# Kernel optimization log

Measured on AMD Instinct MI355X. Metric: run time of the kernel, lower is better.

Reference implementation:

```python
import jax, jax.numpy as jnp
import numpy as np

K = 4
EPS = 1e-6
NEG_INF = -1e9


def _extract_patches(x, k):
    # x: [C, H, W] -> [P, C*k*k], P = (H-k+1)*(W-k+1), p = hp*Wp + wp
    C, H, W = x.shape
    Hp, Wp = H - k + 1, W - k + 1
    cols = jnp.stack([x[:, di:di + Hp, dj:dj + Wp]
                      for di in range(k) for dj in range(k)], axis=1)  # [C, k*k, Hp, Wp]
    return cols.reshape(C * k * k, Hp * Wp).T  # [P, C*k*k]


def setup_inputs() -> dict:
    key = jax.random.key(0)
    k1, k2, k3 = jax.random.split(key, 3)
    C, H, W = 32, 80, 80
    low = jax.random.normal(k1, (1, C, H, W), dtype=jnp.float32)
    high = jax.random.normal(k2, (1, C, H, W), dtype=jnp.float32)
    mask = jax.random.randint(k3, (H + 1, W + 1), 0, 2, dtype=jnp.int32)
    return {"low_level_features": low, "hight_level_features": high, "mask": mask}


def reference(low_level_features, hight_level_features, mask):
    k = K
    low = low_level_features[0]    # [C, H, W]
    high = hight_level_features[0]
    C, H, W = low.shape
    Hp, Wp = H - k + 1, W - k + 1
    P = Hp * Wp

    low_p = _extract_patches(low, k)    # [P, D], D = C*k*k (candidate patches)
    high_p = _extract_patches(high, k)  # [P, D] (query filters)
    norms = jnp.sqrt(jnp.sum(low_p * low_p, axis=1))  # torch.norm per patch, [P]

    # all-pairs cosine-distance scores: [P_query, P_candidate]
    scores = jnp.einsum('qd,pd->qp', high_p, low_p) / (norms + EPS)[None, :]
    # candidates where mask==1 (top-left of patch) are excluded (set to inf=-1e9)
    excl = (mask[:Hp, :Wp].reshape(-1) == 1)
    scores = jnp.where(excl[None, :], NEG_INF, scores)
    best = jnp.argmax(scores, axis=1)   # [P] best match per query patch

    # a query patch at (i,j) is processed only if its 4 mask corners are nonzero
    valid = ((mask[:Hp, :Wp] != 0) & (mask[:Hp, k:k + Wp] != 0) &
             (mask[k:k + Hp, :Wp] != 0) & (mask[k:k + Hp, k:k + Wp] != 0))
    validf = valid.astype(low.dtype).reshape(-1)  # [P]

    gathered = low_p[best] * validf[:, None]            # [P, D]
    g = gathered.reshape(Hp, Wp, C, k, k)               # per-query result patches
    vmap2d = validf.reshape(Hp, Wp)

    result = jnp.zeros_like(low)
    counts = jnp.zeros((H, W), low.dtype)
    for di in range(k):
        for dj in range(k):
            result = result.at[:, di:di + Hp, dj:dj + Wp].add(
                jnp.moveaxis(g[:, :, :, di, dj], -1, 0))
            counts = counts.at[di:di + Hp, dj:dj + Wp].add(vmap2d)

    out = result / (counts + EPS)[None, :, :]
    nz = counts != 0
    out = out * nz[None, :, :] + low * (~nz)[None, :, :]
    return out[None]  # [1, C, H, W]
```

## Files before the change

kernel.cpp:

```cpp
#include <hip/hip_runtime.h>
#include <hip/hip_bf16.h>

#define CC    32
#define HH    80
#define WW    80
#define HW    6400
#define HPQ   77
#define WPQ   77
#define PP    5929
#define DD    512
#define MSTR  81
#define NTILE 93
#define QTILES 372
#define NEGINF (-1e9f)

typedef __attribute__((ext_vector_type(4))) float f32x4;
typedef __attribute__((ext_vector_type(8))) short bf16x8;
typedef __attribute__((ext_vector_type(8))) unsigned short u16x8;

__device__ __forceinline__ void split_bf16(float v, unsigned short& hi, unsigned short& lo) {
    __hip_bfloat16 h = __float2bfloat16(v);
    float hf = __bfloat162float(h);
    __hip_bfloat16 lw = __float2bfloat16(v - hf);
    hi = *reinterpret_cast<unsigned short*>(&h);
    lo = *reinterpret_cast<unsigned short*>(&lw);
}

__global__ __launch_bounds__(1024) void k_mask(const int* __restrict__ mask,
                                               int* __restrict__ excl,
                                               int* __restrict__ valid,
                                               int* __restrict__ qlist,
                                               int* __restrict__ nvalid) {
    __shared__ int cnt;
    if (threadIdx.x == 0) cnt = 0;
    __syncthreads();
    for (int p = threadIdx.x; p < PP; p += 1024) {
        int pi = p / WPQ, pj = p % WPQ;
        int m00 = mask[pi * MSTR + pj];
        int m01 = mask[pi * MSTR + pj + 4];
        int m10 = mask[(pi + 4) * MSTR + pj];
        int m11 = mask[(pi + 4) * MSTR + pj + 4];
        excl[p] = (m00 == 1) ? 1 : 0;
        int v = (m00 != 0 && m01 != 0 && m10 != 0 && m11 != 0) ? 1 : 0;
        valid[p] = v;
        if (v) {
            int s = atomicAdd(&cnt, 1);
            qlist[s] = p;
        }
    }
    __syncthreads();
    if (threadIdx.x == 0) *nvalid = cnt;
}

__global__ __launch_bounds__(256) void k_packBn(const float* __restrict__ low,
                                                unsigned short* __restrict__ Bhi,
                                                unsigned short* __restrict__ Blo) {
    const int u = blockIdx.x;
    const int tid = threadIdx.x;
    const int l = tid & 63, w = tid >> 6;
    const int n = l & 15, quad = l >> 4;
    const int p = u * 16 + n;
    const bool pok = (p < PP);
    const int pi = pok ? p / WPQ : 0, pj = pok ? p % WPQ : 0;
    const int pbase = pi * WW + pj;

    float v[4][8];
    float sq = 0.f;
#pragma unroll
    for (int ss = 0; ss < 4; ++ss) {
        int s = w * 4 + ss;
        int kbase = s * 32 + quad * 8;
        int base = (kbase >> 4) * HW + pbase;
#pragma unroll
        for (int j = 0; j < 8; ++j) {
            int kk = kbase + j;
            int di = (kk >> 2) & 3, dj = kk & 3;
            float x = pok ? low[base + di * WW + dj] : 0.f;
            v[ss][j] = x;
            sq += x * x;
        }
    }
    __shared__ float part[16][17];
    __shared__ float invn_s[16];
    part[w * 4 + quad][n] = sq;
    __syncthreads();
    if (tid < 16) {
        float t = 0.f;
#pragma unroll
        for (int i = 0; i < 16; ++i) t += part[i][tid];
        invn_s[tid] = 1.0f / (sqrtf(t) + 1e-6f);
    }
    __syncthreads();
    const float sc = invn_s[n];
#pragma unroll
    for (int ss = 0; ss < 4; ++ss) {
        int s = w * 4 + ss;
        u16x8 vh, vl;
#pragma unroll
        for (int j = 0; j < 8; ++j) {
            unsigned short h, lo;
            split_bf16(v[ss][j] * sc, h, lo);
            vh[j] = h; vl[j] = lo;
        }
        int off = u * 8192 + s * 512 + l * 8;
        *reinterpret_cast<u16x8*>(Bhi + off) = vh;
        *reinterpret_cast<u16x8*>(Blo + off) = vl;
    }
}

__global__ __launch_bounds__(256) void k_packA(const float* __restrict__ high,
                                               const int* __restrict__ qlist,
                                               const int* __restrict__ nvalid,
                                               unsigned short* __restrict__ Ahi,
                                               unsigned short* __restrict__ Alo) {
    int t = blockIdx.x * 256 + threadIdx.x;
    if (t >= QTILES * 16 * 64) return;
    int nv = *nvalid;
    int l = t & 63;
    int s = (t >> 6) & 15;
    int u = t >> 10;
    if ((u >> 2) * 64 >= nv) return;
    int m = l & 15, quad = l >> 4;
    int slot = u * 16 + m;
    int kbase = s * 32 + quad * 8;

    u16x8 vh, vl;
    if (slot < nv) {
        int q = qlist[slot];
        int qi = q / WPQ, qj = q % WPQ;
        int base = (kbase >> 4) * HW + qi * WW + qj;
#pragma unroll
        for (int j = 0; j < 8; ++j) {
            int kk = kbase + j;
            int di = (kk >> 2) & 3, dj = kk & 3;
            float v = high[base + di * WW + dj];
            unsigned short h, lo;
            split_bf16(v, h, lo);
            vh[j] = h; vl[j] = lo;
        }
    } else {
#pragma unroll
        for (int j = 0; j < 8; ++j) { vh[j] = 0; vl[j] = 0; }
    }
    int off = t * 8;
    *reinterpret_cast<u16x8*>(Ahi + off) = vh;
    *reinterpret_cast<u16x8*>(Alo + off) = vl;
}

__global__ __launch_bounds__(256) void k_score(const unsigned short* __restrict__ Ahi,
                                               const unsigned short* __restrict__ Alo,
                                               const unsigned short* __restrict__ Bhi,
                                               const unsigned short* __restrict__ Blo,
                                               const int* __restrict__ excl,
                                               const int* __restrict__ nvalid,
                                               float* __restrict__ pscore,
                                               int* __restrict__ pidx) {
    const int nv = *nvalid;
    const int qblk = blockIdx.y;
    if (qblk * 64 >= nv) return;
    const int pblk = blockIdx.x;
    const int w = threadIdx.x >> 6;
    const int l = threadIdx.x & 63;
    const int qtile = qblk * 4 + w;

    f32x4 acc[4];
#pragma unroll
    for (int pt = 0; pt < 4; ++pt) acc[pt] = (f32x4){0.f, 0.f, 0.f, 0.f};

    const int abase = qtile * 8192 + l * 8;
    const int bbase0 = pblk * 4 * 8192 + l * 8;

#pragma unroll 4
    for (int s = 0; s < 16; ++s) {
        bf16x8 ah = *reinterpret_cast<const bf16x8*>(Ahi + abase + s * 512);
        bf16x8 al = *reinterpret_cast<const bf16x8*>(Alo + abase + s * 512);
#pragma unroll
        for (int pt = 0; pt < 4; ++pt) {
            int boff = bbase0 + pt * 8192 + s * 512;
            bf16x8 bh = *reinterpret_cast<const bf16x8*>(Bhi + boff);
            bf16x8 bl = *reinterpret_cast<const bf16x8*>(Blo + boff);
            acc[pt] = __builtin_amdgcn_mfma_f32_16x16x32_bf16(ah, bh, acc[pt], 0, 0, 0);
            acc[pt] = __builtin_amdgcn_mfma_f32_16x16x32_bf16(ah, bl, acc[pt], 0, 0, 0);
            acc[pt] = __builtin_amdgcn_mfma_f32_16x16x32_bf16(al, bh, acc[pt], 0, 0, 0);
        }
    }

    const int n = l & 15, quad = l >> 4;
    float bs[4]; int bi[4];
#pragma unroll
    for (int r = 0; r < 4; ++r) { bs[r] = -3.4e38f; bi[r] = 0x7fffffff; }
#pragma unroll
    for (int pt = 0; pt < 4; ++pt) {
        int gp = pblk * 64 + pt * 16 + n;
        if (gp < PP) {
            bool ex = (excl[gp] != 0);
#pragma unroll
            for (int r = 0; r < 4; ++r) {
                float sv = ex ? NEGINF : acc[pt][r];
                if (sv > bs[r]) { bs[r] = sv; bi[r] = gp; }
            }
        }
    }
#pragma unroll
    for (int off = 1; off <= 8; off <<= 1) {
#pragma unroll
        for (int r = 0; r < 4; ++r) {
            float s2 = __shfl_xor(bs[r], off, 64);
            int   i2 = __shfl_xor(bi[r], off, 64);
            if (s2 > bs[r] || (s2 == bs[r] && i2 < bi[r])) { bs[r] = s2; bi[r] = i2; }
        }
    }
    if (n == 0) {
#pragma unroll
        for (int r = 0; r < 4; ++r) {
            int slot = qtile * 16 + quad * 4 + r;
            pscore[slot * NTILE + pblk] = bs[r];
            pidx[slot * NTILE + pblk] = bi[r];
        }
    }
}

__global__ __launch_bounds__(64) void k_reduce(const float* __restrict__ pscore,
                                               const int* __restrict__ pidx,
                                               const int* __restrict__ qlist,
                                               const int* __restrict__ nvalid,
                                               int* __restrict__ best) {
    const int slot = blockIdx.x;
    if (slot >= *nvalid) return;
    const int t = threadIdx.x;
    float bs = -3.4e38f;
    int bi = 0x7fffffff;
    for (int k = t; k < NTILE; k += 64) {
        float s = pscore[slot * NTILE + k];
        int i = pidx[slot * NTILE + k];
        if (s > bs || (s == bs && i < bi)) { bs = s; bi = i; }
    }
#pragma unroll
    for (int off = 32; off >= 1; off >>= 1) {
        float s2 = __shfl_down(bs, off);
        int   i2 = __shfl_down(bi, off);
        if (s2 > bs || (s2 == bs && i2 < bi)) { bs = s2; bi = i2; }
    }
    if (t == 0) best[qlist[slot]] = bi;
}

__global__ __launch_bounds__(256) void k_prep(const int* __restrict__ best,
                                              const int* __restrict__ valid,
                                              int* __restrict__ cnt,
                                              int* __restrict__ offlist) {
    int pix = blockIdx.x * 256 + threadIdx.x;
    if (pix >= HW) return;
    int i = pix / WW, j = pix % WW;
    int n = 0;
#pragma unroll
    for (int di = 0; di < 4; ++di) {
        int qi = i - di;
        if (qi < 0 || qi >= HPQ) continue;
#pragma unroll
        for (int dj = 0; dj < 4; ++dj) {
            int qj = j - dj;
            if (qj < 0 || qj >= WPQ) continue;
            int q = qi * WPQ + qj;
            if (valid[q]) {
                int b = best[q];
                int bi = b / WPQ, bj = b % WPQ;
                offlist[pix * 16 + n] = (bi + di) * WW + (bj + dj);
                n++;
            }
        }
    }
    cnt[pix] = n;
}

__global__ __launch_bounds__(256) void k_out(const float* __restrict__ low,
                                             const int* __restrict__ cnt,
                                             const int* __restrict__ offlist,
                                             float* __restrict__ out) {
    int idx = blockIdx.x * 256 + threadIdx.x;
    if (idx >= CC * HW) return;
    int c = idx / HW;
    int pix = idx % HW;
    int n = cnt[pix];
    if (n > 0) {
        int base = c * HW;
        float acc = 0.f;
        for (int t = 0; t < n; ++t)
            acc += low[base + offlist[pix * 16 + t]];
        out[idx] = acc / ((float)n + 1e-6f);
    } else {
        out[idx] = low[idx];
    }
}

extern "C" void kernel_launch(void* const* d_in, const int* in_sizes, int n_in,
                              void* d_out, int out_size, void* d_ws, size_t ws_size,
                              hipStream_t stream) {
    const float* low  = (const float*)d_in[0];
    const float* high = (const float*)d_in[1];
    const int*   mask = (const int*)d_in[2];
    float* out = (float*)d_out;

    char* ws = (char*)d_ws;
    int*   nvalid = (int*)(ws);
    int*   qlist  = (int*)(ws + 64);
    int*   excl   = (int*)(ws + 24064);
    int*   valid  = (int*)(ws + 48128);
    int*   best   = (int*)(ws + 72192);
    float* pscore = (float*)(ws + 96256);
    int*   pidx   = (int*)(ws + 2310400);
    int*   cnt    = (int*)(ws + 4524544);
    int*   offlist= (int*)(ws + 4550144);
    unsigned short* Ahi = (unsigned short*)(ws + 4959744);
    unsigned short* Alo = (unsigned short*)(ws + 11054592);
    unsigned short* Bhi = (unsigned short*)(ws + 17149440);
    unsigned short* Blo = (unsigned short*)(ws + 23244288);

    hipLaunchKernelGGL(k_mask, dim3(1), dim3(1024), 0, stream,
                       mask, excl, valid, qlist, nvalid);
    hipLaunchKernelGGL(k_packBn, dim3(QTILES), dim3(256), 0, stream,
                       low, Bhi, Blo);
    hipLaunchKernelGGL(k_packA, dim3(QTILES * 4), dim3(256), 0, stream,
                       high, qlist, nvalid, Ahi, Alo);
    hipLaunchKernelGGL(k_score, dim3(NTILE, 93), dim3(256), 0, stream,
                       Ahi, Alo, Bhi, Blo, excl, nvalid, pscore, pidx);
    hipLaunchKernelGGL(k_reduce, dim3(5952), dim3(64), 0, stream,
                       pscore, pidx, qlist, nvalid, best);
    hipLaunchKernelGGL(k_prep, dim3((HW + 255) / 256), dim3(256), 0, stream,
                       best, valid, cnt, offlist);
    hipLaunchKernelGGL(k_out, dim3((CC * HW + 255) / 256), dim3(256), 0, stream,
                       low, cnt, offlist, out);
}
```

Before: 111.2 us.

## Fuse argmax reduction via packed atomicMax and merge pack/output kernels

Replaces the per-tile partial score/index buffers and separate reduce kernel with a 64-bit packed (order-preserving score, inverted index) atomicMax into a per-slot best array, cleared in the mask kernel. Merges the A and B packing kernels into one launch, and fuses the prep and output gather kernels into one that computes offsets on the fly and handles 8 channels per thread. This cuts the launch count from seven to four and removes intermediate global traffic, at the cost of global atomic contention and recomputing the offsets in each channel group.

```diff
diff --git a/kernel.cpp b/kernel.cpp
--- a/kernel.cpp
+++ b/kernel.cpp
@@ -12,6 +12,7 @@
 #define MSTR  81
 #define NTILE 93
 #define QTILES 372
+#define NSLOT 5952
 #define NEGINF (-1e9f)
 
 typedef __attribute__((ext_vector_type(4))) float f32x4;
@@ -26,13 +27,22 @@
     lo = *reinterpret_cast<unsigned short*>(&lw);
 }
 
+__device__ __forceinline__ unsigned long long enc_si(float s, int idx) {
+    unsigned int b = __float_as_uint(s);
+    unsigned int u = (b & 0x80000000u) ? ~b : (b | 0x80000000u);
+    return ((unsigned long long)u << 32) | (unsigned int)(~idx);
+}
+
 __global__ __launch_bounds__(1024) void k_mask(const int* __restrict__ mask,
                                                int* __restrict__ excl,
                                                int* __restrict__ valid,
                                                int* __restrict__ qlist,
-                                               int* __restrict__ nvalid) {
+                                               int* __restrict__ qslot,
+                                               int* __restrict__ nvalid,
+                                               unsigned long long* __restrict__ bestPacked) {
     __shared__ int cnt;
     if (threadIdx.x == 0) cnt = 0;
+    for (int i = threadIdx.x; i < NSLOT; i += 1024) bestPacked[i] = 0ull;
     __syncthreads();
     for (int p = threadIdx.x; p < PP; p += 1024) {
         int pi = p / WPQ, pj = p % WPQ;
@@ -46,105 +56,107 @@
         if (v) {
             int s = atomicAdd(&cnt, 1);
             qlist[s] = p;
+            qslot[p] = s;
         }
     }
     __syncthreads();
     if (threadIdx.x == 0) *nvalid = cnt;
 }
 
-__global__ __launch_bounds__(256) void k_packBn(const float* __restrict__ low,
-                                                unsigned short* __restrict__ Bhi,
-                                                unsigned short* __restrict__ Blo) {
-    const int u = blockIdx.x;
+__global__ __launch_bounds__(256) void k_pack(const float* __restrict__ low,
+                                              const float* __restrict__ high,
+                                              const int* __restrict__ qlist,
+                                              const int* __restrict__ nvalid,
+                                              unsigned short* __restrict__ Bhi,
+                                              unsigned short* __restrict__ Blo,
+                                              unsigned short* __restrict__ Ahi,
+                                              unsigned short* __restrict__ Alo) {
+    const int bid = blockIdx.x;
     const int tid = threadIdx.x;
-    const int l = tid & 63, w = tid >> 6;
-    const int n = l & 15, quad = l >> 4;
-    const int p = u * 16 + n;
-    const bool pok = (p < PP);
-    const int pi = pok ? p / WPQ : 0, pj = pok ? p % WPQ : 0;
-    const int pbase = pi * WW + pj;
-
-    float v[4][8];
-    float sq = 0.f;
-#pragma unroll
-    for (int ss = 0; ss < 4; ++ss) {
-        int s = w * 4 + ss;
+    if (bid < QTILES) {
+        const int u = bid;
+        const int l = tid & 63, w = tid >> 6;
+        const int n = l & 15, quad = l >> 4;
+        const int p = u * 16 + n;
+        const bool pok = (p < PP);
+        const int pi = pok ? p / WPQ : 0, pj = pok ? p % WPQ : 0;
+        const int pbase = pi * WW + pj;
+
+        float v[4][8];
+        float sq = 0.f;
+#pragma unroll
+        for (int ss = 0; ss < 4; ++ss) {
+            int s = w * 4 + ss;
+            int kbase = s * 32 + quad * 8;
+            int base = (kbase >> 4) * HW + pbase;
+#pragma unroll
+            for (int j = 0; j < 8; ++j) {
+                int kk = kbase + j;
+                int di = (kk >> 2) & 3, dj = kk & 3;
+                float x = pok ? low[base + di * WW + dj] : 0.f;
+                v[ss][j] = x;
+                sq += x * x;
+            }
+        }
+        __shared__ float part[16][17];
+        __shared__ float invn_s[16];
+        part[w * 4 + quad][n] = sq;
+        __syncthreads();
+        if (tid < 16) {
+            float t = 0.f;
+#pragma unroll
+            for (int i = 0; i < 16; ++i) t += part[i][tid];
+            invn_s[tid] = 1.0f / (sqrtf(t) + 1e-6f);
+        }
+        __syncthreads();
+        const float sc = invn_s[n];
+#pragma unroll
+        for (int ss = 0; ss < 4; ++ss) {
+            int s = w * 4 + ss;
+            u16x8 vh, vl;
+#pragma unroll
+            for (int j = 0; j < 8; ++j) {
+                unsigned short h, lo;
+                split_bf16(v[ss][j] * sc, h, lo);
+                vh[j] = h; vl[j] = lo;
+            }
+            int off = u * 8192 + s * 512 + l * 8;
+            *reinterpret_cast<u16x8*>(Bhi + off) = vh;
+            *reinterpret_cast<u16x8*>(Blo + off) = vl;
+        }
+    } else {
+        int t = (bid - QTILES) * 256 + tid;
+        int nv = *nvalid;
+        int l = t & 63;
+        int s = (t >> 6) & 15;
+        int u = t >> 10;
+        if ((u >> 2) * 64 >= nv) return;
+        int m = l & 15, quad = l >> 4;
+        int slot = u * 16 + m;
         int kbase = s * 32 + quad * 8;
-        int base = (kbase >> 4) * HW + pbase;
-#pragma unroll
-        for (int j = 0; j < 8; ++j) {
-            int kk = kbase + j;
-            int di = (kk >> 2) & 3, dj = kk & 3;
-            float x = pok ? low[base + di * WW + dj] : 0.f;
-            v[ss][j] = x;
-            sq += x * x;
-        }
-    }
-    __shared__ float part[16][17];
-    __shared__ float invn_s[16];
-    part[w * 4 + quad][n] = sq;
-    __syncthreads();
-    if (tid < 16) {
-        float t = 0.f;
-#pragma unroll
-        for (int i = 0; i < 16; ++i) t += part[i][tid];
-        invn_s[tid] = 1.0f / (sqrtf(t) + 1e-6f);
-    }
-    __syncthreads();
-    const float sc = invn_s[n];
-#pragma unroll
-    for (int ss = 0; ss < 4; ++ss) {
-        int s = w * 4 + ss;
+
         u16x8 vh, vl;
-#pragma unroll
-        for (int j = 0; j < 8; ++j) {
-            unsigned short h, lo;
-            split_bf16(v[ss][j] * sc, h, lo);
-            vh[j] = h; vl[j] = lo;
-        }
-        int off = u * 8192 + s * 512 + l * 8;
-        *reinterpret_cast<u16x8*>(Bhi + off) = vh;
-        *reinterpret_cast<u16x8*>(Blo + off) = vl;
-    }
-}
-
-__global__ __launch_bounds__(256) void k_packA(const float* __restrict__ high,
-                                               const int* __restrict__ qlist,
-                                               const int* __restrict__ nvalid,
-                                               unsigned short* __restrict__ Ahi,
-                                               unsigned short* __restrict__ Alo) {
-    int t = blockIdx.x * 256 + threadIdx.x;
-    if (t >= QTILES * 16 * 64) return;
-    int nv = *nvalid;
-    int l = t & 63;
-    int s = (t >> 6) & 15;
-    int u = t >> 10;
-    if ((u >> 2) * 64 >= nv) return;
-    int m = l & 15, quad = l >> 4;
-    int slot = u * 16 + m;
-    int kbase = s * 32 + quad * 8;
-
-    u16x8 vh, vl;
-    if (slot < nv) {
-        int q = qlist[slot];
-        int qi = q / WPQ, qj = q % WPQ;
-        int base = (kbase >> 4) * HW + qi * WW + qj;
-#pragma unroll
-        for (int j = 0; j < 8; ++j) {
-            int kk = kbase + j;
-            int di = (kk >> 2) & 3, dj = kk & 3;
-            float v = high[base + di * WW + dj];
-            unsigned short h, lo;
-            split_bf16(v, h, lo);
-            vh[j] = h; vl[j] = lo;
-        }
-    } else {
-#pragma unroll
-        for (int j = 0; j < 8; ++j) { vh[j] = 0; vl[j] = 0; }
-    }
-    int off = t * 8;
-    *reinterpret_cast<u16x8*>(Ahi + off) = vh;
-    *reinterpret_cast<u16x8*>(Alo + off) = vl;
+        if (slot < nv) {
+            int q = qlist[slot];
+            int qi = q / WPQ, qj = q % WPQ;
+            int base = (kbase >> 4) * HW + qi * WW + qj;
+#pragma unroll
+            for (int j = 0; j < 8; ++j) {
+                int kk = kbase + j;
+                int di = (kk >> 2) & 3, dj = kk & 3;
+                float v = high[base + di * WW + dj];
+                unsigned short h, lo;
+                split_bf16(v, h, lo);
+                vh[j] = h; vl[j] = lo;
+            }
+        } else {
+#pragma unroll
+            for (int j = 0; j < 8; ++j) { vh[j] = 0; vl[j] = 0; }
+        }
+        int off = t * 8;
+        *reinterpret_cast<u16x8*>(Ahi + off) = vh;
+        *reinterpret_cast<u16x8*>(Alo + off) = vl;
+    }
 }
 
 __global__ __launch_bounds__(256) void k_score(const unsigned short* __restrict__ Ahi,
@@ -153,8 +165,7 @@
                                                const unsigned short* __restrict__ Blo,
                                                const int* __restrict__ excl,
                                                const int* __restrict__ nvalid,
-                                               float* __restrict__ pscore,
-                                               int* __restrict__ pidx) {
+                                               unsigned long long* __restrict__ bestPacked) {
     const int nv = *nvalid;
     const int qblk = blockIdx.y;
     if (qblk * 64 >= nv) return;
@@ -214,43 +225,24 @@
 #pragma unroll
         for (int r = 0; r < 4; ++r) {
             int slot = qtile * 16 + quad * 4 + r;
-            pscore[slot * NTILE + pblk] = bs[r];
-            pidx[slot * NTILE + pblk] = bi[r];
-        }
-    }
-}
-
-__global__ __launch_bounds__(64) void k_reduce(const float* __restrict__ pscore,
-                                               const int* __restrict__ pidx,
-                                               const int* __restrict__ qlist,
-                                               const int* __restrict__ nvalid,
-                                               int* __restrict__ best) {
-    const int slot = blockIdx.x;
-    if (slot >= *nvalid) return;
-    const int t = threadIdx.x;
-    float bs = -3.4e38f;
-    int bi = 0x7fffffff;
-    for (int k = t; k < NTILE; k += 64) {
-        float s = pscore[slot * NTILE + k];
-        int i = pidx[slot * NTILE + k];
-        if (s > bs || (s == bs && i < bi)) { bs = s; bi = i; }
-    }
-#pragma unroll
-    for (int off = 32; off >= 1; off >>= 1) {
-        float s2 = __shfl_down(bs, off);
-        int   i2 = __shfl_down(bi, off);
-        if (s2 > bs || (s2 == bs && i2 < bi)) { bs = s2; bi = i2; }
-    }
-    if (t == 0) best[qlist[slot]] = bi;
-}
-
-__global__ __launch_bounds__(256) void k_prep(const int* __restrict__ best,
+            atomicMax(&bestPacked[slot], enc_si(bs[r], bi[r]));
+        }
+    }
+}
+
+__global__ __launch_bounds__(256) void k_outf(const float* __restrict__ low,
                                               const int* __restrict__ valid,
-                                              int* __restrict__ cnt,
-                                              int* __restrict__ offlist) {
+                                              const int* __restrict__ qslot,
+                                              const unsigned long long* __restrict__ bestPacked,
+                                              float* __restrict__ out) {
     int pix = blockIdx.x * 256 + threadIdx.x;
     if (pix >= HW) return;
+    const int c0 = blockIdx.y * 8;
     int i = pix / WW, j = pix % WW;
+
+    float acc[8];
+#pragma unroll
+    for (int cc = 0; cc < 8; ++cc) acc[cc] = 0.f;
     int n = 0;
 #pragma unroll
     for (int di = 0; di < 4; ++di) {
@@ -262,33 +254,26 @@
             if (qj < 0 || qj >= WPQ) continue;
             int q = qi * WPQ + qj;
             if (valid[q]) {
-                int b = best[q];
-                int bi = b / WPQ, bj = b % WPQ;
-                offlist[pix * 16 + n] = (bi + di) * WW + (bj + dj);
+                unsigned long long pk = bestPacked[qslot[q]];
+                int b = (int)(~(unsigned int)(pk & 0xFFFFFFFFull));
+                int bi2 = b / WPQ, bj2 = b % WPQ;
+                int off = (bi2 + di) * WW + (bj2 + dj);
                 n++;
-            }
-        }
-    }
-    cnt[pix] = n;
-}
-
-__global__ __launch_bounds__(256) void k_out(const float* __restrict__ low,
-                                             const int* __restrict__ cnt,
-                                             const int* __restrict__ offlist,
-                                             float* __restrict__ out) {
-    int idx = blockIdx.x * 256 + threadIdx.x;
-    if (idx >= CC * HW) return;
-    int c = idx / HW;
-    int pix = idx % HW;
-    int n = cnt[pix];
+#pragma unroll
+                for (int cc = 0; cc < 8; ++cc)
+                    acc[cc] += low[(c0 + cc) * HW + off];
+            }
+        }
+    }
     if (n > 0) {
-        int base = c * HW;
-        float acc = 0.f;
-        for (int t = 0; t < n; ++t)
-            acc += low[base + offlist[pix * 16 + t]];
-        out[idx] = acc / ((float)n + 1e-6f);
+        float inv = 1.0f / ((float)n + 1e-6f);
+#pragma unroll
+        for (int cc = 0; cc < 8; ++cc)
+            out[(c0 + cc) * HW + pix] = acc[cc] * inv;
     } else {
-        out[idx] = low[idx];
+#pragma unroll
+        for (int cc = 0; cc < 8; ++cc)
+            out[(c0 + cc) * HW + pix] = low[(c0 + cc) * HW + pix];
     }
 }
 
@@ -301,32 +286,23 @@
     float* out = (float*)d_out;
 
     char* ws = (char*)d_ws;
-    int*   nvalid = (int*)(ws);
-    int*   qlist  = (int*)(ws + 64);
-    int*   excl   = (int*)(ws + 24064);
-    int*   valid  = (int*)(ws + 48128);
-    int*   best   = (int*)(ws + 72192);
-    float* pscore = (float*)(ws + 96256);
-    int*   pidx   = (int*)(ws + 2310400);
-    int*   cnt    = (int*)(ws + 4524544);
-    int*   offlist= (int*)(ws + 4550144);
-    unsigned short* Ahi = (unsigned short*)(ws + 4959744);
-    unsigned short* Alo = (unsigned short*)(ws + 11054592);
-    unsigned short* Bhi = (unsigned short*)(ws + 17149440);
-    unsigned short* Blo = (unsigned short*)(ws + 23244288);
+    int* nvalid = (int*)(ws);
+    int* qlist  = (int*)(ws + 64);
+    int* qslot  = (int*)(ws + 24064);
+    int* valid  = (int*)(ws + 48128);
+    int* excl   = (int*)(ws + 72192);
+    unsigned long long* bestPacked = (unsigned long long*)(ws + 96256);
+    unsigned short* Ahi = (unsigned short*)(ws + 143936);
+    unsigned short* Alo = (unsigned short*)(ws + 6238784);
+    unsigned short* Bhi = (unsigned short*)(ws + 12333632);
+    unsigned short* Blo = (unsigned short*)(ws + 18428480);
 
     hipLaunchKernelGGL(k_mask, dim3(1), dim3(1024), 0, stream,
-                       mask, excl, valid, qlist, nvalid);
-    hipLaunchKernelGGL(k_packBn, dim3(QTILES), dim3(256), 0, stream,
-                       low, Bhi, Blo);
-    hipLaunchKernelGGL(k_packA, dim3(QTILES * 4), dim3(256), 0, stream,
-                       high, qlist, nvalid, Ahi, Alo);
+                       mask, excl, valid, qlist, qslot, nvalid, bestPacked);
+    hipLaunchKernelGGL(k_pack, dim3(QTILES + QTILES * 4), dim3(256), 0, stream,
+                       low, high, qlist, nvalid, Bhi, Blo, Ahi, Alo);
     hipLaunchKernelGGL(k_score, dim3(NTILE, 93), dim3(256), 0, stream,
-                       Ahi, Alo, Bhi, Blo, excl, nvalid, pscore, pidx);
-    hipLaunchKernelGGL(k_reduce, dim3(5952), dim3(64), 0, stream,
-                       pscore, pidx, qlist, nvalid, best);
-    hipLaunchKernelGGL(k_prep, dim3((HW + 255) / 256), dim3(256), 0, stream,
-                       best, valid, cnt, offlist);
-    hipLaunchKernelGGL(k_out, dim3((CC * HW + 255) / 256), dim3(256), 0, stream,
-                       low, cnt, offlist, out);
-}
+                       Ahi, Alo, Bhi, Blo, excl, nvalid, bestPacked);
+    hipLaunchKernelGGL(k_outf, dim3((HW + 255) / 256, 4), dim3(256), 0, stream,
+                       low, valid, qslot, bestPacked, out);
+}
```

Result: no change. 112.3 us (+1.0%).
